# Kernel optimization log

Hardware: AMD Instinct MI355X
Metric: run time of the kernel (lower is better)

Reference implementation:

```python
import jax, jax.numpy as jnp
import numpy as np

N, L, S, C, H = 4, 2048, 4096, 256, 8
D = C // H          # head dim = 32
HID = 4 * C         # mlp hidden = 1024
LN_EPS = 1e-5
LA_EPS = 1e-6


def _layer_norm(x, g, b):
    m = x.mean(-1, keepdims=True)
    v = ((x - m) ** 2).mean(-1, keepdims=True)
    return (x - m) * jax.lax.rsqrt(v + LN_EPS) * g + b


def _linear_attention(q, k, v):
    # q: [N,L,H,D], k/v: [N,S,H,D]  (elu feature map linear attention)
    Q = jax.nn.elu(q) + 1.0
    K = jax.nn.elu(k) + 1.0
    v_len = v.shape[1]
    KV = jnp.einsum('nshd,nshv->nhdv', K, v / v_len)
    Z = 1.0 / (jnp.einsum('nlhd,nhd->nlh', Q, K.sum(axis=1)) + LA_EPS)
    return jnp.einsum('nlhd,nhdv,nlh->nlhv', Q, KV, Z) * v_len


def setup_inputs() -> dict:
    key = jax.random.key(0)
    ks = jax.random.split(key, 32)
    f32 = jnp.float32
    w = lambda k, *s: (jax.random.normal(k, s, dtype=f32) * 0.02)
    inp = {
        'tgt': jax.random.normal(ks[0], (N, L, C), dtype=f32),
        'memory': jax.random.normal(ks[1], (N, S, C), dtype=f32),
        'tgt_pos': jax.random.normal(ks[2], (N, L, C), dtype=f32),
        'pos_embed': w(ks[3], 1, S, C),
        # layer norms
        'ln1_g': jnp.ones((C,), f32), 'ln1_b': jnp.zeros((C,), f32),
        'ln2_g': jnp.ones((C,), f32), 'ln2_b': jnp.zeros((C,), f32),
        'ln3_g': jnp.ones((C,), f32), 'ln3_b': jnp.zeros((C,), f32),
        # self-attn projections (stored (in,out))
        'wq': w(ks[4], C, C), 'bq': jnp.zeros((C,), f32),
        'wk': w(ks[5], C, C), 'bk': jnp.zeros((C,), f32),
        'wv': w(ks[6], C, C), 'bv': jnp.zeros((C,), f32),
        'w_merge': w(ks[7], C, C),
        # cross-attn (CCAttention) projections
        'cwq': w(ks[8], C, C), 'cbq': jnp.zeros((C,), f32),
        'cwk': w(ks[9], C, C), 'cbk': jnp.zeros((C,), f32),
        'cwv': w(ks[10], C, C), 'cbv': jnp.zeros((C,), f32),
        'cwo': w(ks[11], C, C), 'cbo': jnp.zeros((C,), f32),
        # mlp (fc1 -> dwconv3x3 -> gelu -> fc2)
        'mw1': w(ks[12], C, HID), 'mb1': jnp.zeros((HID,), f32),
        'dw_k': w(ks[13], HID, 1, 3, 3), 'dw_b': jnp.zeros((HID,), f32),
        'mw2': w(ks[14], HID, C), 'mb2': jnp.zeros((C,), f32),
        'num_points': L,
    }
    return inp


def reference(tgt, memory, tgt_pos, pos_embed,
              ln1_g, ln1_b, ln2_g, ln2_b, ln3_g, ln3_b,
              wq, bq, wk, bk, wv, bv, w_merge,
              cwq, cbq, cwk, cbk, cwv, cbv, cwo, cbo,
              mw1, mb1, dw_k, dw_b, mw2, mb2, num_points):
    n, l, c = tgt.shape
    # ---- self attention (linear attention) ----
    tgt2 = _layer_norm(tgt, ln1_g, ln1_b)
    qk = tgt2 + tgt_pos
    q = (qk @ wq + bq).reshape(n, l, H, D)
    k = (qk @ wk + bk).reshape(n, l, H, D)
    v = (tgt2 @ wv + bv).reshape(n, l, H, D)
    msg = _linear_attention(q, k, v).reshape(n, l, c) @ w_merge
    tgt = tgt + msg  # dropout is identity in eval
    # ---- cross attention (CCAttention, softmax MHA) ----
    tgt2 = _layer_norm(tgt, ln2_g, ln2_b)
    mem = memory + pos_embed
    cq = (tgt2 @ cwq + cbq).reshape(n, l, H, D)
    ck = (mem @ cwk + cbk).reshape(n, -1, H, D)
    cv = (mem @ cwv + cbv).reshape(n, -1, H, D)
    scale = D ** -0.5
    attn = jax.nn.softmax(jnp.einsum('nlhd,nshd->nhls', cq, ck) * scale, axis=-1)
    cmsg = jnp.einsum('nhls,nshd->nlhd', attn, cv).reshape(n, l, c) @ cwo + cbo
    tgt = tgt + cmsg
    # ---- MLP with depthwise conv over (num_points, 1) grid ----
    x = _layer_norm(tgt, ln3_g, ln3_b)
    h = x @ mw1 + mb1                                   # [n,l,HID]
    hi = h.transpose(0, 2, 1).reshape(n, HID, num_points, 1)
    hi = jax.lax.conv_general_dilated(
        hi, dw_k, window_strides=(1, 1), padding=((1, 1), (1, 1)),
        feature_group_count=HID,
        dimension_numbers=('NCHW', 'OIHW', 'NCHW'))
    hi = hi + dw_b[None, :, None, None]
    h = hi.reshape(n, HID, l).transpose(0, 2, 1)
    h = jax.nn.gelu(h, approximate=False)
    mlp_out = h @ mw2 + mb2
    return tgt + mlp_out
```

## Files before the change

kernel.cpp:

```cpp
#include <hip/hip_runtime.h>
#include <hip/hip_bf16.h>
#include <math.h>

#define NB 4
#define LL 2048
#define SS 4096
#define CC 256
#define HH 8
#define DD 32
#define HIDN 1024
#define NSPLIT 4
#define DWROWS 8

using bf16 = __hip_bfloat16;
typedef __attribute__((ext_vector_type(8))) short short8;
typedef __attribute__((ext_vector_type(4))) short short4v;
typedef __attribute__((ext_vector_type(4))) float floatx4;

__device__ __forceinline__ float b2f(bf16 x) { return __bfloat162float(x); }
__device__ __forceinline__ short f2bs(float x) {
    bf16 h = __float2bfloat16(x);
    return *(short*)&h;
}
__device__ __forceinline__ short f2bs_fast(float x) {
    return (short)(__float_as_uint(x) >> 16);
}
__device__ __forceinline__ float s2f(short s) {
    bf16 h = *(bf16*)&s;
    return __bfloat162float(h);
}

#if __has_builtin(__builtin_amdgcn_exp2f)
#define EXP2(x) __builtin_amdgcn_exp2f(x)
#else
#define EXP2(x) exp2f(x)
#endif

__device__ __forceinline__ bool probe_f32(const unsigned* p) {
    return p[0] == 0x3F800000u;
}
__device__ __forceinline__ float ldx(const void* p, size_t i, bool f32m) {
    return f32m ? ((const float*)p)[i] : b2f(((const bf16*)p)[i]);
}
__device__ __forceinline__ void ldx4(const void* p, size_t i, bool f32m, float* x) {
    if (f32m) {
        float4 v = *(const float4*)((const float*)p + i);
        x[0] = v.x; x[1] = v.y; x[2] = v.z; x[3] = v.w;
    } else {
        short4v s = *(const short4v*)((const short*)p + i);
        #pragma unroll
        for (int j = 0; j < 4; ++j) x[j] = s2f(s[j]);
    }
}

struct WPack { const void* p[10]; };

__global__ __launch_bounds__(256)
void wprep_kernel(WPack pk, short* __restrict__ dst, float* __restrict__ zbuf,
                  const unsigned* __restrict__ probe) {
    const int z = blockIdx.z;
    const int tid = threadIdx.x;
    if (z == 10) {
        int idx = (blockIdx.y * 16 + blockIdx.x) * 256 + tid;
        if (idx < 35072) zbuf[idx] = 0.0f;
        return;
    }
    const bool f32m = probe_f32(probe);
    const int K = (z == 9) ? 1024 : 256;
    const int N = (z == 8) ? 1024 : 256;
    const size_t off = (z < 8) ? (size_t)z * 65536 : (z == 8 ? 524288u : 786432u);
    const int k0 = blockIdx.y * 64, n0 = blockIdx.x * 64;
    if (k0 >= K || n0 >= N) return;
    __shared__ float T[64][65];
    const void* src = pk.p[z];
    #pragma unroll
    for (int p = 0; p < 16; ++p) {
        int idx = tid + p * 256;
        int r = idx >> 6, c = idx & 63;
        T[r][c] = ldx(src, (size_t)(k0 + r) * N + n0 + c, f32m);
    }
    __syncthreads();
    short* d = dst + off;
    #pragma unroll
    for (int p = 0; p < 16; ++p) {
        int idx = tid + p * 256;
        int c2 = idx >> 6, r2 = idx & 63;
        d[(size_t)(n0 + c2) * K + k0 + r2] = f2bs(T[r2][c2]);
    }
}

__global__ __launch_bounds__(256)
void ln_kernel(const void* __restrict__ xr, const float* __restrict__ xf,
               const void* __restrict__ g, const void* __restrict__ bta,
               const void* __restrict__ pos,
               short* __restrict__ y, short* __restrict__ y2,
               const unsigned* __restrict__ probe) {
    const bool f32m = probe_f32(probe);
    const int w = threadIdx.x >> 6, lane = threadIdx.x & 63;
    const int row = blockIdx.x * 4 + w;
    const int c0 = lane * 4;
    const size_t base = (size_t)row * CC;
    float x[4];
    if (xr) ldx4(xr, base + c0, f32m, x);
    else {
        float4 v = *(const float4*)(xf + base + c0);
        x[0] = v.x; x[1] = v.y; x[2] = v.z; x[3] = v.w;
    }
    float a = x[0] + x[1] + x[2] + x[3];
    float b = x[0]*x[0] + x[1]*x[1] + x[2]*x[2] + x[3]*x[3];
    #pragma unroll
    for (int off = 1; off < 64; off <<= 1) {
        a += __shfl_xor(a, off);
        b += __shfl_xor(b, off);
    }
    const float mean = a * (1.0f / CC);
    const float var = b * (1.0f / CC) - mean * mean;
    const float inv = rsqrtf(var + 1e-5f);
    float yv[4];
    short r[4];
    #pragma unroll
    for (int j = 0; j < 4; ++j) {
        yv[j] = (x[j] - mean) * inv * ldx(g, c0 + j, f32m) + ldx(bta, c0 + j, f32m);
        r[j] = f2bs(yv[j]);
    }
    *(short4v*)&y[base + c0] = short4v{r[0], r[1], r[2], r[3]};
    if (y2) {
        float pz[4];
        ldx4(pos, base + c0, f32m, pz);
        short r2[4];
        #pragma unroll
        for (int j = 0; j < 4; ++j) r2[j] = f2bs(yv[j] + pz[j]);
        *(short4v*)&y2[base + c0] = short4v{r2[0], r2[1], r2[2], r2[3]};
    }
}

__global__ __launch_bounds__(256)
void ln_addpos_kernel(const float* __restrict__ xf, const void* __restrict__ g,
                      const void* __restrict__ bta, short* __restrict__ y,
                      const void* __restrict__ mem, const void* __restrict__ pos,
                      short* __restrict__ memout,
                      const unsigned* __restrict__ probe) {
    const bool f32m = probe_f32(probe);
    const int w = threadIdx.x >> 6, lane = threadIdx.x & 63;
    int row = blockIdx.x * 4 + w;
    const int c0 = lane * 4;
    if (row >= NB * LL) {
        row -= NB * LL;
        const int s = row & (SS - 1);
        float m[4], p[4];
        ldx4(mem, (size_t)row * CC + c0, f32m, m);
        ldx4(pos, (size_t)s * CC + c0, f32m, p);
        short r[4];
        #pragma unroll
        for (int j = 0; j < 4; ++j) r[j] = f2bs(m[j] + p[j]);
        *(short4v*)&memout[(size_t)row * CC + c0] = short4v{r[0], r[1], r[2], r[3]};
        return;
    }
    const size_t base = (size_t)row * CC;
    float4 v = *(const float4*)(xf + base + c0);
    float x[4] = {v.x, v.y, v.z, v.w};
    float a = x[0] + x[1] + x[2] + x[3];
    float b = x[0]*x[0] + x[1]*x[1] + x[2]*x[2] + x[3]*x[3];
    #pragma unroll
    for (int off = 1; off < 64; off <<= 1) {
        a += __shfl_xor(a, off);
        b += __shfl_xor(b, off);
    }
    const float mean = a * (1.0f / CC);
    const float var = b * (1.0f / CC) - mean * mean;
    const float inv = rsqrtf(var + 1e-5f);
    short r[4];
    #pragma unroll
    for (int j = 0; j < 4; ++j)
        r[j] = f2bs((x[j] - mean) * inv * ldx(g, c0 + j, f32m) + ldx(bta, c0 + j, f32m));
    *(short4v*)&y[base + c0] = short4v{r[0], r[1], r[2], r[3]};
}

template <int BM, int BN>
__device__ __forceinline__
void gemm_body(const short* __restrict__ A, const short* __restrict__ Bt,
               const void* bias, const void* bias2,
               const float* __restrict__ residF, const void* __restrict__ residR,
               void* Cout, void* Cout2,
               int N, int K, bool f32m, int epi, int outmode, int transc2,
               int bx, int by) {
    constexpr int WM = BM / 2, AI = WM / 16;
    constexpr int WN = BN / 2, BJ = WN / 16;
    constexpr int ACH = (BM == 128) ? 4 : 2;
    constexpr int BCH = (BN == 128) ? 4 : 2;
    __shared__ __attribute__((aligned(16))) short As[2][BM][72];
    __shared__ __attribute__((aligned(16))) short Bs[2][BN][72];
    const int tid = threadIdx.x;
    const int ln = tid & 15, quad = (tid >> 4) & 3, w = tid >> 6;
    const int wm = (w & 1) * WM, wn = (w >> 1) * WN;
    const int bm = by * BM, bn = bx * BN;
    const int ar = (BM == 128) ? (tid >> 1) : (tid >> 2);
    const int ac = (BM == 128) ? ((tid & 1) * 32) : ((tid & 3) * 16);
    const int br = (BN == 128) ? (tid >> 1) : (tid >> 2);
    const int bc = (BN == 128) ? ((tid & 1) * 32) : ((tid & 3) * 16);

    short8 pa[ACH], pb[BCH];
    {
        const short* ag = &A[(size_t)(bm + ar) * K + ac];
        #pragma unroll
        for (int t = 0; t < ACH; ++t) pa[t] = *(const short8*)(ag + t * 8);
        const short* bg = &Bt[(size_t)(bn + br) * K + bc];
        #pragma unroll
        for (int t = 0; t < BCH; ++t) pb[t] = *(const short8*)(bg + t * 8);
    }
    floatx4 acc[AI][BJ] = {};
    const int NK = K >> 6;
    for (int it = 0; it < NK; ++it) {
        const int buf = it & 1;
        #pragma unroll
        for (int t = 0; t < ACH; ++t) *(short8*)&As[buf][ar][ac + t * 8] = pa[t];
        #pragma unroll
        for (int t = 0; t < BCH; ++t) *(short8*)&Bs[buf][br][bc + t * 8] = pb[t];
        if (it + 1 < NK) {
            const int k1 = (it + 1) << 6;
            const short* ag = &A[(size_t)(bm + ar) * K + k1 + ac];
            #pragma unroll
            for (int t = 0; t < ACH; ++t) pa[t] = *(const short8*)(ag + t * 8);
            const short* bg = &Bt[(size_t)(bn + br) * K + k1 + bc];
            #pragma unroll
            for (int t = 0; t < BCH; ++t) pb[t] = *(const short8*)(bg + t * 8);
        }
        __syncthreads();
        #pragma unroll
        for (int ks = 0; ks < 2; ++ks) {
            short8 af[AI], bf[BJ];
            #pragma unroll
            for (int i = 0; i < AI; ++i)
                af[i] = *(const short8*)&As[buf][wm + i * 16 + ln][ks * 32 + quad * 8];
            #pragma unroll
            for (int j = 0; j < BJ; ++j)
                bf[j] = *(const short8*)&Bs[buf][wn + j * 16 + ln][ks * 32 + quad * 8];
            #pragma unroll
            for (int i = 0; i < AI; ++i)
                #pragma unroll
                for (int j = 0; j < BJ; ++j)
                    acc[i][j] = __builtin_amdgcn_mfma_f32_16x16x32_bf16(af[i], bf[j], acc[i][j], 0, 0, 0);
        }
    }
    #pragma unroll
    for (int i = 0; i < AI; ++i)
        #pragma unroll
        for (int j = 0; j < BJ; ++j) {
            const int gr0 = bm + wm + i * 16 + quad * 4;
            const int gc = bn + wn + j * 16 + ln;
            const bool hi = (Cout2 != nullptr) && (gc >= 256);
            const int col = hi ? gc - 256 : gc;
            const int sN = Cout2 ? 256 : N;
            void* co = hi ? Cout2 : Cout;
            const void* bb = hi ? bias2 : bias;
            float vv[4];
            #pragma unroll
            for (int r = 0; r < 4; ++r) {
                float v = acc[i][j][r];
                if (bb) v += ldx(bb, col, f32m);
                if (epi == 1) v = (v > 0.0f) ? (v + 1.0f) : __expf(v);
                const size_t o = (size_t)(gr0 + r) * sN + col;
                if (residF) v += residF[o];
                if (residR) v += ldx(residR, o, f32m);
                vv[r] = v;
            }
            if (transc2 && hi) {
                const int nb = gr0 >> 12;
                const int s = gr0 & (SS - 1);
                short4v pk4 = {f2bs(vv[0]), f2bs(vv[1]), f2bs(vv[2]), f2bs(vv[3])};
                *(short4v*)&((short*)co)[((size_t)nb * CC + col) * SS + s] = pk4;
            } else {
                #pragma unroll
                for (int r = 0; r < 4; ++r) {
                    const size_t o = (size_t)(gr0 + r) * sN + col;
                    if (outmode == 0) ((float*)co)[o] = vv[r];
                    else if (outmode == 2) ((short*)co)[o] = f2bs(vv[r]);
                    else {
                        if (f32m) ((float*)co)[o] = vv[r];
                        else      ((bf16*)co)[o] = __float2bfloat16(vv[r]);
                    }
                }
            }
        }
}

template <int BM, int BN, int EPI, int OUTMODE, int TRANSC2>
__global__ __launch_bounds__(256)
void gemm_mfma_kernel(const short* __restrict__ A, const short* __restrict__ Bt,
                      const void* __restrict__ bias, const void* __restrict__ bias2,
                      const float* __restrict__ residF, const void* __restrict__ residR,
                      void* __restrict__ Cout, void* __restrict__ Cout2,
                      int M, int N, int K, const unsigned* __restrict__ probe) {
    (void)M;
    gemm_body<BM, BN>(A, Bt, bias, bias2, residF, residR, Cout, Cout2,
                      N, K, probe_f32(probe), EPI, OUTMODE, TRANSC2,
                      blockIdx.x, blockIdx.y);
}

__global__ __launch_bounds__(256)
void gemm_qkv_kernel(const short* __restrict__ qkA, const short* __restrict__ wqkT,
                     const void* bq, const void* bk,
                     float* __restrict__ phiq, float* __restrict__ phik,
                     const short* __restrict__ vA, const short* __restrict__ wvT,
                     const void* bv, float* __restrict__ vout,
                     const unsigned* __restrict__ probe) {
    const bool f32m = probe_f32(probe);
    const bool second = blockIdx.x >= 8;
    gemm_body<64, 64>(second ? vA : qkA,
                      second ? wvT : wqkT,
                      second ? bv : bq,
                      second ? nullptr : bk,
                      nullptr, nullptr,
                      second ? (void*)vout : (void*)phiq,
                      second ? nullptr : (void*)phik,
                      second ? 256 : 512, 256, f32m,
                      second ? 0 : 1, 0, 0,
                      second ? (int)blockIdx.x - 8 : (int)blockIdx.x, blockIdx.y);
}

__global__ __launch_bounds__(256)
void gemm_cqckcv_kernel(const short* __restrict__ lnA, const short* __restrict__ cwqT,
                        const void* cbq, short* __restrict__ cqout,
                        const short* __restrict__ memA, const short* __restrict__ cwkvT,
                        const void* cbk, const void* cbv,
                        short* __restrict__ ckout, short* __restrict__ cvTout,
                        const unsigned* __restrict__ probe) {
    const bool f32m = probe_f32(probe);
    const bool second = blockIdx.x >= 4;
    if (!second && blockIdx.y >= (NB * LL) / 64) return;
    gemm_body<64, 64>(second ? memA : lnA,
                      second ? cwkvT : cwqT,
                      second ? cbk : cbq,
                      second ? cbv : nullptr,
                      nullptr, nullptr,
                      second ? (void*)ckout : (void*)cqout,
                      second ? (void*)cvTout : nullptr,
                      second ? 512 : 256, 256, f32m,
                      0, 2, second ? 1 : 0,
                      second ? (int)blockIdx.x - 4 : (int)blockIdx.x, blockIdx.y);
}

#define KVSPLIT 16
__global__ __launch_bounds__(256)
void linattn_kv_kernel(const float* __restrict__ Kp, const float* __restrict__ Vp,
                       float* __restrict__ KV, float* __restrict__ Ksum) {
    const int h = blockIdx.x, n = blockIdx.y, z = blockIdx.z;
    __shared__ __attribute__((aligned(16))) float Kt[64][33];
    __shared__ __attribute__((aligned(16))) float Vt[64][32];
    const int tid = threadIdx.x;
    const int d = tid >> 3, e0 = (tid & 7) * 4;
    const int sbeg = z * (LL / KVSPLIT), send = sbeg + (LL / KVSPLIT);
    float acc[4] = {}, ks = 0.0f;
    for (int s0 = sbeg; s0 < send; s0 += 64) {
        #pragma unroll
        for (int p = 0; p < 8; ++p) {
            int idx = tid + p * 256;
            int r = idx >> 5, c = idx & 31;
            size_t gaddr = (size_t)((n * LL) + s0 + r) * CC + h * DD + c;
            Kt[r][c] = Kp[gaddr];
            Vt[r][c] = Vp[gaddr];
        }
        __syncthreads();
        for (int s = 0; s < 64; ++s) {
            float kd = Kt[s][d];
            ks += kd;
            float4 v4 = *(const float4*)&Vt[s][e0];
            acc[0] += kd * v4.x; acc[1] += kd * v4.y;
            acc[2] += kd * v4.z; acc[3] += kd * v4.w;
        }
        __syncthreads();
    }
    float* kvp = &KV[(size_t)((n * HH + h) * DD + d) * DD + e0];
    atomicAdd(&kvp[0], acc[0]); atomicAdd(&kvp[1], acc[1]);
    atomicAdd(&kvp[2], acc[2]); atomicAdd(&kvp[3], acc[3]);
    if ((tid & 7) == 0) atomicAdd(&Ksum[(n * HH + h) * DD + d], ks);
}

__global__ __launch_bounds__(256)
void linattn_out_kernel(const float* __restrict__ Qp, const float* __restrict__ KV,
                        const float* __restrict__ Ksum, short* __restrict__ Out) {
    const int lt = blockIdx.x, h = blockIdx.y, n = blockIdx.z;
    __shared__ float KVs[32][33];
    __shared__ float Ks[32];
    __shared__ float Qs[64][33];
    const int tid = threadIdx.x;
    for (int p = 0; p < 4; ++p) {
        int idx = tid + p * 256;
        KVs[idx >> 5][idx & 31] = KV[(size_t)(n * HH + h) * (DD * DD) + idx];
    }
    if (tid < 32) Ks[tid] = Ksum[(n * HH + h) * DD + tid];
    for (int p = 0; p < 8; ++p) {
        int idx = tid + p * 256;
        int r = idx >> 5, c = idx & 31;
        Qs[r][c] = Qp[(size_t)((n * LL) + lt * 64 + r) * CC + h * DD + c];
    }
    __syncthreads();
    const int e = tid & 31;
    for (int ii = 0; ii < 8; ++ii) {
        const int i = (tid >> 5) + ii * 8;
        float num = 0.0f, den = 0.0f;
        for (int d = 0; d < 32; ++d) {
            float q = Qs[i][d];
            num += q * KVs[d][e];
            den += q * Ks[d];
        }
        Out[(size_t)((n * LL) + lt * 64 + i) * CC + h * DD + e] = f2bs(num / (den + 1e-6f));
    }
}

__global__ __launch_bounds__(256)
void flash_mfma_kernel(const short* __restrict__ Q, const short* __restrict__ K,
                       const short* __restrict__ V,
                       float* __restrict__ Of, float* __restrict__ Lp, int zoff) {
    const int lt = blockIdx.x, h = blockIdx.y;
    const int z = blockIdx.z + zoff;
    const int n = z / NSPLIT, sp = z % NSPLIT;
    const int tid = threadIdx.x;
    const int ln = tid & 15;
    const int quad = (tid >> 4) & 3;
    const int w = tid >> 6;
    const int NT = NB * LL;
    const float qscale = 0.17677669529663687f * 1.4426950408889634f;

    __shared__ __attribute__((aligned(16))) short Ks[2][64][40];
    __shared__ __attribute__((aligned(16))) short Vp[2][32][72];

    short8 bQa, bQb;
    {
        const size_t qrow = (size_t)(n * LL) + lt * 128 + w * 16 + ln;
        short8 qv0 = *(const short8*)&Q[qrow * CC + h * DD + quad * 8];
        short8 qv1 = *(const short8*)&Q[(qrow + 64) * CC + h * DD + quad * 8];
        short t0[8], t1[8];
        #pragma unroll
        for (int j = 0; j < 8; ++j) {
            t0[j] = f2bs(s2f(qv0[j]) * qscale);
            t1[j] = f2bs(s2f(qv1[j]) * qscale);
        }
        bQa = *(short8*)t0;
        bQb = *(short8*)t1;
    }

    const short one_b = (short)0x3F80;
    const short8 ones8 = {one_b, one_b, one_b, one_b, one_b, one_b, one_b, one_b};

    floatx4 o0a = {0.f, 0.f, 0.f, 0.f}, o1a = {0.f, 0.f, 0.f, 0.f};
    floatx4 o2a = {0.f, 0.f, 0.f, 0.f};
    floatx4 o0b = {0.f, 0.f, 0.f, 0.f}, o1b = {0.f, 0.f, 0.f, 0.f};
    floatx4 o2b = {0.f, 0.f, 0.f, 0.f};
    const floatx4 zinit = {-24.f, -24.f, -24.f, -24.f};

    const int r_st = tid >> 2, c0_st = (tid & 3) * 8;
    const int e_st = tid >> 3, m_st = tid & 7;
    const int K32 = (m_st >> 2) * 32;
    const int h4 = ((m_st >> 1) & 1) * 4;
    const int q0s = (2 * m_st) & 3;
    const int slotA = K32 + q0s * 8 + h4;
    const int slotB = K32 + (q0s + 1) * 8 + h4;

    const int sbeg = sp * (SS / NSPLIT);
    constexpr int NIT = (SS / NSPLIT) / 64;

    const short* kptr = &K[(size_t)((n * SS) + sbeg + r_st) * CC + h * DD + c0_st];
    const short* vptr = &V[((size_t)n * CC + h * DD + e_st) * SS + sbeg + m_st * 8];
    short8 kreg = *(const short8*)kptr;
    short8 vreg = *(const short8*)vptr;

    for (int it = 0; it < NIT; ++it) {
        const int buf = it & 1;
        *(short8*)&Ks[buf][r_st][c0_st] = kreg;
        {
            short4v lo = {vreg[0], vreg[1], vreg[2], vreg[3]};
            short4v hi = {vreg[4], vreg[5], vreg[6], vreg[7]};
            *(short4v*)&Vp[buf][e_st][slotA] = lo;
            *(short4v*)&Vp[buf][e_st][slotB] = hi;
        }
        if (it + 1 < NIT) {
            kreg = *(const short8*)(kptr + (size_t)(it + 1) * 64 * CC);
            vreg = *(const short8*)(vptr + (it + 1) * 64);
        }
        __syncthreads();

        floatx4 sa[4], sb[4];
        #pragma unroll
        for (int g = 0; g < 4; ++g) {
            short8 aK = *(const short8*)&Ks[buf][g * 16 + ln][quad * 8];
            sa[g] = __builtin_amdgcn_mfma_f32_16x16x32_bf16(aK, bQa, zinit, 0, 0, 0);
            sb[g] = __builtin_amdgcn_mfma_f32_16x16x32_bf16(aK, bQb, zinit, 0, 0, 0);
        }

        #pragma unroll
        for (int ks = 0; ks < 2; ++ks) {
            union { unsigned u[4]; short8 s8; } ca, cb;
            #pragma unroll
            for (int jj = 0; jj < 4; ++jj) {
                const int j0 = 2 * jj, j1 = 2 * jj + 1;
                float pa0 = EXP2(sa[2 * ks + (j0 >> 2)][j0 & 3]);
                float pa1 = EXP2(sa[2 * ks + (j1 >> 2)][j1 & 3]);
                ca.u[jj] = __builtin_amdgcn_perm(
                    __float_as_uint(pa1), __float_as_uint(pa0), 0x07060302u);
                float pb0 = EXP2(sb[2 * ks + (j0 >> 2)][j0 & 3]);
                float pb1 = EXP2(sb[2 * ks + (j1 >> 2)][j1 & 3]);
                cb.u[jj] = __builtin_amdgcn_perm(
                    __float_as_uint(pb1), __float_as_uint(pb0), 0x07060302u);
            }
            short8 bV0 = *(const short8*)&Vp[buf][ln][ks * 32 + quad * 8];
            short8 bV1 = *(const short8*)&Vp[buf][16 + ln][ks * 32 + quad * 8];
            o0a = __builtin_amdgcn_mfma_f32_16x16x32_bf16(ca.s8, bV0, o0a, 0, 0, 0);
            o1a = __builtin_amdgcn_mfma_f32_16x16x32_bf16(ca.s8, bV1, o1a, 0, 0, 0);
            o2a = __builtin_amdgcn_mfma_f32_16x16x32_bf16(ca.s8, ones8, o2a, 0, 0, 0);
            o0b = __builtin_amdgcn_mfma_f32_16x16x32_bf16(cb.s8, bV0, o0b, 0, 0, 0);
            o1b = __builtin_amdgcn_mfma_f32_16x16x32_bf16(cb.s8, bV1, o1b, 0, 0, 0);
            o2b = __builtin_amdgcn_mfma_f32_16x16x32_bf16(cb.s8, ones8, o2b, 0, 0, 0);
        }
    }

    const int rb_a = lt * 128 + w * 16;
    const int rb_b = rb_a + 64;
    if (ln == 0) {
        #pragma unroll
        for (int r = 0; r < 4; ++r) {
            Lp[((size_t)sp * NT + (size_t)n * LL + rb_a + quad * 4 + r) * HH + h] = o2a[r];
            Lp[((size_t)sp * NT + (size_t)n * LL + rb_b + quad * 4 + r) * HH + h] = o2b[r];
        }
    }
    #pragma unroll
    for (int r = 0; r < 4; ++r) {
        {
            const size_t row = (size_t)n * LL + rb_a + quad * 4 + r;
            float* o = &Of[((size_t)sp * NT + row) * CC + h * DD];
            o[ln] = o0a[r];
            o[16 + ln] = o1a[r];
        }
        {
            const size_t row = (size_t)n * LL + rb_b + quad * 4 + r;
            float* o = &Of[((size_t)sp * NT + row) * CC + h * DD];
            o[ln] = o0b[r];
            o[16 + ln] = o1b[r];
        }
    }
}

__global__ __launch_bounds__(256)
void flash_merge_kernel(const float* __restrict__ Of, const float* __restrict__ Lp,
                        short* __restrict__ O) {
    const int row = blockIdx.x, c = threadIdx.x, h = c >> 5;
    const size_t NT = (size_t)NB * LL;
    float l = 0.0f, v = 0.0f;
    #pragma unroll
    for (int sp = 0; sp < NSPLIT; ++sp) {
        l += Lp[((size_t)sp * NT + row) * HH + h];
        v += Of[((size_t)sp * NT + row) * CC + c];
    }
    O[(size_t)row * CC + c] = f2bs(v / l);
}

__global__ __launch_bounds__(256)
void dwconv_gelu_kernel(const short* __restrict__ H1, const void* __restrict__ wk,
                        const void* __restrict__ wb, short* __restrict__ H2,
                        const unsigned* __restrict__ probe) {
    const bool f32m = probe_f32(probe);
    const int row0 = blockIdx.x * DWROWS;
    const int l0 = row0 & (LL - 1);
    const int c0 = threadIdx.x * 4;
    float wm[4], w0[4], wp[4], bb[4];
    #pragma unroll
    for (int j = 0; j < 4; ++j) {
        const int ch = c0 + j;
        wm[j] = ldx(wk, ch * 9 + 1, f32m);
        w0[j] = ldx(wk, ch * 9 + 4, f32m);
        wp[j] = ldx(wk, ch * 9 + 7, f32m);
        bb[j] = ldx(wb, ch, f32m);
    }
    const short* base = &H1[(size_t)row0 * HIDN + c0];
    short4v xm = {}, xc;
    if (l0 > 0) xm = *(const short4v*)(base - HIDN);
    xc = *(const short4v*)base;
    #pragma unroll
    for (int i = 0; i < DWROWS; ++i) {
        const int l = l0 + i;
        short4v xp = {};
        if (l < LL - 1) xp = *(const short4v*)(base + (size_t)(i + 1) * HIDN);
        short r[4];
        #pragma unroll
        for (int j = 0; j < 4; ++j) {
            float v = s2f(xm[j]) * wm[j] + s2f(xc[j]) * w0[j] + s2f(xp[j]) * wp[j] + bb[j];
            r[j] = f2bs(0.5f * v * (1.0f + erff(v * 0.70710678118654752f)));
        }
        *(short4v*)&H2[(size_t)(row0 + i) * HIDN + c0] = short4v{r[0], r[1], r[2], r[3]};
        xm = xc; xc = xp;
    }
}

extern "C" void kernel_launch(void* const* d_in, const int* in_sizes, int n_in,
                              void* d_out, int out_size, void* d_ws, size_t ws_size,
                              hipStream_t stream) {
    const void* tgt      = d_in[0];
    const void* memory   = d_in[1];
    const void* tgt_pos  = d_in[2];
    const void* pos_emb  = d_in[3];
    const void* ln1_g = d_in[4],  *ln1_b = d_in[5];
    const void* ln2_g = d_in[6],  *ln2_b = d_in[7];
    const void* ln3_g = d_in[8],  *ln3_b = d_in[9];
    const void* wq = d_in[10], *bq = d_in[11];
    const void* wk = d_in[12], *bk = d_in[13];
    const void* wv = d_in[14], *bv = d_in[15];
    const void* w_merge = d_in[16];
    const void* cwq = d_in[17], *cbq = d_in[18];
    const void* cwk = d_in[19], *cbk = d_in[20];
    const void* cwv = d_in[21], *cbv = d_in[22];
    const void* cwo = d_in[23], *cbo = d_in[24];
    const void* mw1 = d_in[25], *mb1 = d_in[26];
    const void* dw_k = d_in[27], *dw_b = d_in[28];
    const void* mw2 = d_in[29], *mb2 = d_in[30];
    const unsigned* probe = (const unsigned*)d_in[4];

    char* w = (char*)d_ws;
    const size_t MB = 1024 * 1024;
    short* lnout_b = (short*)(w + 0 * MB);
    short* qk_b    = (short*)(w + 4 * MB);
    float* Tbuf    = (float*)(w + 8 * MB);
    float* phiq    = (float*)(w + 16 * MB);
    float* phik    = (float*)(w + 24 * MB);
    float* vbuf    = (float*)(w + 32 * MB);
    float* KVb     = (float*)(w + 40 * MB);
    float* Ksb     = (float*)(w + 40 * MB + 131072);
    float* Ofb     = (float*)(w + 16 * MB);
    float* Lpb     = (float*)(w + 48 * MB);
    short* cqbuf   = (short*)(w + 49 * MB);
    short* membuf  = (short*)(w + 53 * MB);
    short* ckbuf   = (short*)(w + 61 * MB);
    short* cvT     = (short*)(w + 69 * MB);
    short* flashO  = (short*)(w + 77 * MB);
    short* wT      = (short*)(w + 81 * MB);
    short* H1      = (short*)(w + 16 * MB);
    short* H2      = (short*)(w + 32 * MB);

    short* wqT  = wT + 0 * 65536;
    short* wvT  = wT + 2 * 65536;
    short* wmT  = wT + 3 * 65536;
    short* cwqT = wT + 4 * 65536;
    short* cwkT = wT + 5 * 65536;
    short* cwoT = wT + 7 * 65536;
    short* mw1T = wT + 524288;
    short* mw2T = wT + 786432;

    const int NT = NB * LL;
    const int NS = NB * SS;
    const dim3 blk(256);

    WPack pk;
    pk.p[0] = wq;  pk.p[1] = wk;  pk.p[2] = wv;  pk.p[3] = w_merge;
    pk.p[4] = cwq; pk.p[5] = cwk; pk.p[6] = cwv; pk.p[7] = cwo;
    pk.p[8] = mw1; pk.p[9] = mw2;
    wprep_kernel<<<dim3(16, 16, 11), blk, 0, stream>>>(pk, wT, KVb, probe);

    ln_kernel<<<NT / 4, blk, 0, stream>>>(tgt, nullptr, ln1_g, ln1_b, tgt_pos, lnout_b, qk_b, probe);
    gemm_qkv_kernel<<<dim3(12, NT / 64), blk, 0, stream>>>(
        qk_b, wqT, bq, bk, phiq, phik, lnout_b, wvT, bv, vbuf, probe);
    linattn_kv_kernel<<<dim3(HH, NB, KVSPLIT), blk, 0, stream>>>(phik, vbuf, KVb, Ksb);
    linattn_out_kernel<<<dim3(LL / 64, HH, NB), blk, 0, stream>>>(phiq, KVb, Ksb, (short*)vbuf);
    gemm_mfma_kernel<64, 64, 0, 0, 0><<<dim3(4, NT / 64), blk, 0, stream>>>(
        (short*)vbuf, wmT, nullptr, nullptr, nullptr, tgt, Tbuf, nullptr, NT, CC, CC, probe);

    ln_addpos_kernel<<<(NT + NS) / 4, blk, 0, stream>>>(
        Tbuf, ln2_g, ln2_b, lnout_b, memory, pos_emb, membuf, probe);
    gemm_cqckcv_kernel<<<dim3(12, NS / 64), blk, 0, stream>>>(
        lnout_b, cwqT, cbq, cqbuf, membuf, cwkT, cbk, cbv, ckbuf, cvT, probe);
    flash_mfma_kernel<<<dim3(LL / 128, HH, NB * NSPLIT / 2), blk, 0, stream>>>(
        cqbuf, ckbuf, cvT, Ofb, Lpb, 0);
    flash_mfma_kernel<<<dim3(LL / 128, HH, NB * NSPLIT / 2), blk, 0, stream>>>(
        cqbuf, ckbuf, cvT, Ofb, Lpb, NB * NSPLIT / 2);
    flash_merge_kernel<<<NT, blk, 0, stream>>>(Ofb, Lpb, flashO);
    gemm_mfma_kernel<64, 64, 0, 0, 0><<<dim3(4, NT / 64), blk, 0, stream>>>(
        flashO, cwoT, cbo, nullptr, Tbuf, nullptr, Tbuf, nullptr, NT, CC, CC, probe);

    ln_kernel<<<NT / 4, blk, 0, stream>>>(nullptr, Tbuf, ln3_g, ln3_b, nullptr, lnout_b, nullptr, probe);
    gemm_mfma_kernel<64, 64, 0, 2, 0><<<dim3(16, NT / 64), blk, 0, stream>>>(
        lnout_b, mw1T, mb1, nullptr, nullptr, nullptr, H1, nullptr, NT, HIDN, CC, probe);
    dwconv_gelu_kernel<<<NT / DWROWS, blk, 0, stream>>>(H1, dw_k, dw_b, H2, probe);
    gemm_mfma_kernel<64, 64, 0, 1, 0><<<dim3(4, NT / 64), blk, 0, stream>>>(
        H2, mw2T, mb2, nullptr, Tbuf, nullptr, d_out, nullptr, NT, CC, HIDN, probe);

    (void)in_sizes; (void)n_in; (void)out_size; (void)ws_size;
}
```

Measured before the change: 378.0 us.

## Fuse first layernorm into weight prep, shrink GEMM tiles, merge flash launches

Moves the first layernorm (plus the tgt_pos add) into extra z-slices of the weight-prep kernel, removing one launch. Adds BM=32 support to the GEMM body and uses 32x64 tiles for the three N=256 output GEMMs, doubling block count to fill more compute units. Combines the two split flash-attention launches into one launch over all splits. The smaller tiles trade more blocks for less B-tile reuse per block.

Result: faster. 359.7 us (median of 2 runs) (-4.8%).

```diff
diff --git a/kernel.cpp b/kernel.cpp
--- a/kernel.cpp
+++ b/kernel.cpp
@@ -57,6 +57,9 @@
 
 __global__ __launch_bounds__(256)
 void wprep_kernel(WPack pk, short* __restrict__ dst, float* __restrict__ zbuf,
+                  const void* __restrict__ tgt, const void* __restrict__ tgt_pos,
+                  const void* __restrict__ g1, const void* __restrict__ b1,
+                  short* __restrict__ ln_y, short* __restrict__ ln_y2,
                   const unsigned* __restrict__ probe) {
     const int z = blockIdx.z;
     const int tid = threadIdx.x;
@@ -66,6 +69,37 @@
         return;
     }
     const bool f32m = probe_f32(probe);
+    if (z >= 11) {
+        const int w = tid >> 6, lane = tid & 63;
+        const int blk = (z - 11) * 256 + blockIdx.y * 16 + blockIdx.x;
+        const int row = blk * 4 + w;
+        const int c0 = lane * 4;
+        const size_t base = (size_t)row * CC;
+        float x[4];
+        ldx4(tgt, base + c0, f32m, x);
+        float a = x[0] + x[1] + x[2] + x[3];
+        float b = x[0]*x[0] + x[1]*x[1] + x[2]*x[2] + x[3]*x[3];
+        #pragma unroll
+        for (int off = 1; off < 64; off <<= 1) {
+            a += __shfl_xor(a, off);
+            b += __shfl_xor(b, off);
+        }
+        const float mean = a * (1.0f / CC);
+        const float var = b * (1.0f / CC) - mean * mean;
+        const float inv = rsqrtf(var + 1e-5f);
+        float yv[4], pz[4];
+        short r[4], r2[4];
+        ldx4(tgt_pos, base + c0, f32m, pz);
+        #pragma unroll
+        for (int j = 0; j < 4; ++j) {
+            yv[j] = (x[j] - mean) * inv * ldx(g1, c0 + j, f32m) + ldx(b1, c0 + j, f32m);
+            r[j] = f2bs(yv[j]);
+            r2[j] = f2bs(yv[j] + pz[j]);
+        }
+        *(short4v*)&ln_y[base + c0] = short4v{r[0], r[1], r[2], r[3]};
+        *(short4v*)&ln_y2[base + c0] = short4v{r2[0], r2[1], r2[2], r2[3]};
+        return;
+    }
     const int K = (z == 9) ? 1024 : 256;
     const int N = (z == 8) ? 1024 : 256;
     const size_t off = (z < 8) ? (size_t)z * 65536 : (z == 8 ? 524288u : 786432u);
@@ -186,18 +220,20 @@
                int bx, int by) {
     constexpr int WM = BM / 2, AI = WM / 16;
     constexpr int WN = BN / 2, BJ = WN / 16;
-    constexpr int ACH = (BM == 128) ? 4 : 2;
-    constexpr int BCH = (BN == 128) ? 4 : 2;
+    constexpr int ACH = BM / 32;
+    constexpr int BCH = BN / 32;
     __shared__ __attribute__((aligned(16))) short As[2][BM][72];
     __shared__ __attribute__((aligned(16))) short Bs[2][BN][72];
     const int tid = threadIdx.x;
     const int ln = tid & 15, quad = (tid >> 4) & 3, w = tid >> 6;
     const int wm = (w & 1) * WM, wn = (w >> 1) * WN;
     const int bm = by * BM, bn = bx * BN;
-    const int ar = (BM == 128) ? (tid >> 1) : (tid >> 2);
-    const int ac = (BM == 128) ? ((tid & 1) * 32) : ((tid & 3) * 16);
-    const int br = (BN == 128) ? (tid >> 1) : (tid >> 2);
-    const int bc = (BN == 128) ? ((tid & 1) * 32) : ((tid & 3) * 16);
+    const int ar = (BM == 128) ? (tid >> 1) : ((BM == 64) ? (tid >> 2) : (tid >> 3));
+    const int ac = (BM == 128) ? ((tid & 1) * 32)
+                 : ((BM == 64) ? ((tid & 3) * 16) : ((tid & 7) * 8));
+    const int br = (BN == 128) ? (tid >> 1) : ((BN == 64) ? (tid >> 2) : (tid >> 3));
+    const int bc = (BN == 128) ? ((tid & 1) * 32)
+                 : ((BN == 64) ? ((tid & 3) * 16) : ((tid & 7) * 8));
 
     short8 pa[ACH], pb[BCH];
     {
@@ -652,33 +688,31 @@
     pk.p[0] = wq;  pk.p[1] = wk;  pk.p[2] = wv;  pk.p[3] = w_merge;
     pk.p[4] = cwq; pk.p[5] = cwk; pk.p[6] = cwv; pk.p[7] = cwo;
     pk.p[8] = mw1; pk.p[9] = mw2;
-    wprep_kernel<<<dim3(16, 16, 11), blk, 0, stream>>>(pk, wT, KVb, probe);
-
-    ln_kernel<<<NT / 4, blk, 0, stream>>>(tgt, nullptr, ln1_g, ln1_b, tgt_pos, lnout_b, qk_b, probe);
+    wprep_kernel<<<dim3(16, 16, 19), blk, 0, stream>>>(
+        pk, wT, KVb, tgt, tgt_pos, ln1_g, ln1_b, lnout_b, qk_b, probe);
+
     gemm_qkv_kernel<<<dim3(12, NT / 64), blk, 0, stream>>>(
         qk_b, wqT, bq, bk, phiq, phik, lnout_b, wvT, bv, vbuf, probe);
     linattn_kv_kernel<<<dim3(HH, NB, KVSPLIT), blk, 0, stream>>>(phik, vbuf, KVb, Ksb);
     linattn_out_kernel<<<dim3(LL / 64, HH, NB), blk, 0, stream>>>(phiq, KVb, Ksb, (short*)vbuf);
-    gemm_mfma_kernel<64, 64, 0, 0, 0><<<dim3(4, NT / 64), blk, 0, stream>>>(
+    gemm_mfma_kernel<32, 64, 0, 0, 0><<<dim3(4, NT / 32), blk, 0, stream>>>(
         (short*)vbuf, wmT, nullptr, nullptr, nullptr, tgt, Tbuf, nullptr, NT, CC, CC, probe);
 
     ln_addpos_kernel<<<(NT + NS) / 4, blk, 0, stream>>>(
         Tbuf, ln2_g, ln2_b, lnout_b, memory, pos_emb, membuf, probe);
     gemm_cqckcv_kernel<<<dim3(12, NS / 64), blk, 0, stream>>>(
         lnout_b, cwqT, cbq, cqbuf, membuf, cwkT, cbk, cbv, ckbuf, cvT, probe);
-    flash_mfma_kernel<<<dim3(LL / 128, HH, NB * NSPLIT / 2), blk, 0, stream>>>(
+    flash_mfma_kernel<<<dim3(LL / 128, HH, NB * NSPLIT), blk, 0, stream>>>(
         cqbuf, ckbuf, cvT, Ofb, Lpb, 0);
-    flash_mfma_kernel<<<dim3(LL / 128, HH, NB * NSPLIT / 2), blk, 0, stream>>>(
-        cqbuf, ckbuf, cvT, Ofb, Lpb, NB * NSPLIT / 2);
     flash_merge_kernel<<<NT, blk, 0, stream>>>(Ofb, Lpb, flashO);
-    gemm_mfma_kernel<64, 64, 0, 0, 0><<<dim3(4, NT / 64), blk, 0, stream>>>(
+    gemm_mfma_kernel<32, 64, 0, 0, 0><<<dim3(4, NT / 32), blk, 0, stream>>>(
         flashO, cwoT, cbo, nullptr, Tbuf, nullptr, Tbuf, nullptr, NT, CC, CC, probe);
 
     ln_kernel<<<NT / 4, blk, 0, stream>>>(nullptr, Tbuf, ln3_g, ln3_b, nullptr, lnout_b, nullptr, probe);
     gemm_mfma_kernel<64, 64, 0, 2, 0><<<dim3(16, NT / 64), blk, 0, stream>>>(
         lnout_b, mw1T, mb1, nullptr, nullptr, nullptr, H1, nullptr, NT, HIDN, CC, probe);
     dwconv_gelu_kernel<<<NT / DWROWS, blk, 0, stream>>>(H1, dw_k, dw_b, H2, probe);
-    gemm_mfma_kernel<64, 64, 0, 1, 0><<<dim3(4, NT / 64), blk, 0, stream>>>(
+    gemm_mfma_kernel<32, 64, 0, 1, 0><<<dim3(4, NT / 32), blk, 0, stream>>>(
         H2, mw2T, mb2, nullptr, Tbuf, nullptr, d_out, nullptr, NT, CC, HIDN, probe);
 
     (void)in_sizes; (void)n_in; (void)out_size; (void)ws_size;
```
